# Optimization experiments

Hardware: AMD Instinct MI355X
Metric: run time of the kernel (lower is better)

The kernel has to match this reference:

```python
import jax, jax.numpy as jnp
import numpy as np

THRESHOLD = 0.5
MAX_POINTS = 10000
NORMALIZE = True
BIDIRECTIONAL = True
INF = jnp.float32(1e30)


def _voxels_to_points(vox):
    # vox: (D, H, W). Returns padded points (MAX_POINTS, 3) and validity mask.
    D, H, W = vox.shape
    flat = vox.reshape(-1)
    active = flat > THRESHOLD
    n_active = jnp.sum(active.astype(jnp.int32))
    # Stable argsort puts active voxel indices first (deterministic stand-in
    # for torch's randperm subsampling when n_active > MAX_POINTS).
    order = jnp.argsort(jnp.where(active, 0, 1).astype(jnp.int32))
    idx = order[:MAX_POINTS]
    valid = jnp.arange(MAX_POINTS) < jnp.minimum(n_active, MAX_POINTS)
    d = idx // (H * W)
    h = (idx // W) % H
    w = idx % W
    pts = jnp.stack([d, h, w], axis=-1).astype(jnp.float32)  # (MAX_POINTS, 3)
    if NORMALIZE:
        pts = pts / (D - 1) * 2.0 - 1.0
    pts = jnp.where(valid[:, None], pts, 0.0)
    return pts, valid


def _chamfer_single(p1, v1, p2, v2):
    # p1: (N,3), p2: (M,3) padded; v1/v2 are validity masks.
    n1 = jnp.sum(p1 * p1, axis=1)  # (N,)
    n2 = jnp.sum(p2 * p2, axis=1)  # (M,)
    dist = n1[:, None] + n2[None, :] - 2.0 * (p1 @ p2.T)  # (N, M)
    dist = jnp.maximum(dist, 0.0)
    c1 = jnp.maximum(jnp.sum(v1.astype(jnp.float32)), 1.0)
    c2 = jnp.maximum(jnp.sum(v2.astype(jnp.float32)), 1.0)
    min_1to2 = jnp.min(jnp.where(v2[None, :], dist, INF), axis=1)  # (N,)
    loss = jnp.sum(jnp.where(v1, min_1to2, 0.0)) / c1
    if BIDIRECTIONAL:
        min_2to1 = jnp.min(jnp.where(v1[:, None], dist, INF), axis=0)  # (M,)
        loss = loss + jnp.sum(jnp.where(v2, min_2to1, 0.0)) / c2
    return loss


def setup_inputs() -> dict:
    key = jax.random.key(0)
    k1, k2 = jax.random.split(key)
    pred = jax.random.uniform(k1, (4, 1, 64, 64, 64), dtype=jnp.float32)
    target = jax.random.uniform(k2, (4, 1, 64, 64, 64), dtype=jnp.float32)
    return {"pred": pred, "target": target}


def reference(pred, target):
    B = pred.shape[0]
    total = jnp.float32(0.0)
    n_valid = jnp.float32(0.0)
    for b in range(B):  # small fixed batch loop (per-sample dist matrix is 10k x 10k)
        p1, v1 = _voxels_to_points(pred[b, 0])
        p2, v2 = _voxels_to_points(target[b, 0])
        has_pts = jnp.logical_and(jnp.any(v1), jnp.any(v2))
        cd = _chamfer_single(p1, v1, p2, v2)
        total = total + jnp.where(has_pts, cd, 0.0)
        n_valid = n_valid + has_pts.astype(jnp.float32)
    return jnp.where(n_valid > 0, total / jnp.maximum(n_valid, 1.0), 0.0)
```

## Files before the change

kernel.cpp:

```cpp
#include <hip/hip_runtime.h>
#include <hip/hip_bf16.h>


#define NVOX      262144
#define NCHUNK    256
#define MAXPTS    10000
#define PTS_PAD   10240
#define NCLOUD    8
#define NTASK     8
#define NRB       40
#define QPB       256
#define NQB       40
#define RSPLIT    4
#define RLEN      2560
#define CH_REFS   1280
#define CH_STEPS  20
#define NCH       2
#define SCALE     (2.0f/63.0f)

typedef _Float16 half8  __attribute__((ext_vector_type(8)));
typedef float    f32x16 __attribute__((ext_vector_type(16)));

#define WS_TOTALS   0
#define WS_COUNTS   1024
#define WS_OFFSETS  16384
#define WS_QFRAG    32768
#define WS_RFRAG    1343488
#define WS_NQ       2654208
#define WS_SMIN     2981888
#define WS_BSUM     4292608

__device__ __forceinline__ const float* cloud_src(const float* pred, const float* tgt, int cloud) {
    const float* base = (cloud & 1) ? tgt : pred;
    return base + (size_t)(cloud >> 1) * NVOX;
}

__global__ void k_init(half8* __restrict__ Qfrag, half8* __restrict__ Rfrag,
                       float* __restrict__ nqint) {
    int i = blockIdx.x * 256 + threadIdx.x;
    half8 zq = {0, 0, 0, 0, 0, 0, 0, 0};
    half8 zr = {0, 0, 0, (_Float16)4096, 0, 0, 0, 0};
    Qfrag[i] = zq;
    Rfrag[i] = zr;
    nqint[i] = 0.f;
}

__global__ void k_count(const float* __restrict__ pred, const float* __restrict__ tgt,
                        int* __restrict__ counts) {
    int cloud = blockIdx.x >> 8;
    int chunk = blockIdx.x & 255;
    int t = threadIdx.x;
    const float* src = cloud_src(pred, tgt, cloud) + chunk * 1024;
    float4 v = reinterpret_cast<const float4*>(src)[t];
    int cnt = (v.x > 0.5f) + (v.y > 0.5f) + (v.z > 0.5f) + (v.w > 0.5f);
    __shared__ int s[256];
    s[t] = cnt; __syncthreads();
    for (int o = 128; o > 0; o >>= 1) {
        if (t < o) s[t] += s[t + o];
        __syncthreads();
    }
    if (t == 0) counts[cloud * NCHUNK + chunk] = s[0];
}

__global__ void k_scan(const int* __restrict__ counts, int* __restrict__ offsets,
                       int* __restrict__ totals) {
    int cloud = blockIdx.x;
    int t = threadIdx.x;
    int c = counts[cloud * NCHUNK + t];
    __shared__ int s[256];
    s[t] = c; __syncthreads();
    for (int o = 1; o < 256; o <<= 1) {
        int v = (t >= o) ? s[t - o] : 0;
        __syncthreads();
        s[t] += v;
        __syncthreads();
    }
    offsets[cloud * NCHUNK + t] = s[t] - c;
    if (t == 255) totals[cloud] = s[255];
}

__global__ void k_compact(const float* __restrict__ pred, const float* __restrict__ tgt,
                          const int* __restrict__ offsets,
                          half8* __restrict__ Qfrag, half8* __restrict__ Rfrag,
                          float* __restrict__ nqint) {
    int cloud = blockIdx.x >> 8;
    int chunk = blockIdx.x & 255;
    int t = threadIdx.x;
    const float* src = cloud_src(pred, tgt, cloud) + chunk * 1024;
    float4 v = reinterpret_cast<const float4*>(src)[t];
    int f0 = v.x > 0.5f, f1 = v.y > 0.5f, f2 = v.z > 0.5f, f3 = v.w > 0.5f;
    int cnt = f0 + f1 + f2 + f3;
    __shared__ int s[256];
    s[t] = cnt; __syncthreads();
    for (int o = 1; o < 256; o <<= 1) {
        int x = (t >= o) ? s[t - o] : 0;
        __syncthreads();
        s[t] += x;
        __syncthreads();
    }
    int rank = offsets[cloud * NCHUNK + chunk] + (s[t] - cnt);
    int eidx = chunk * 1024 + t * 4;
    int flags[4] = {f0, f1, f2, f3};
    size_t base = (size_t)cloud * PTS_PAD;
    #pragma unroll
    for (int e = 0; e < 4; ++e) {
        if (flags[e]) {
            if (rank < MAXPTS) {
                int idx = eidx + e;
                int d = idx >> 12, h = (idx >> 6) & 63, w = idx & 63;
                int nr = d * d + h * h + w * w;
                half8 Q = {(_Float16)(-2 * d), (_Float16)(-2 * h), (_Float16)(-2 * w),
                           (_Float16)8, (_Float16)1, 0, 0, 0};
                half8 R = {(_Float16)d, (_Float16)h, (_Float16)w,
                           (_Float16)(nr >> 3), (_Float16)(nr & 7), 0, 0, 0};
                Qfrag[base + rank] = Q;
                Rfrag[base + rank] = R;
                nqint[base + rank] = (float)nr;
            }
            rank++;
        }
    }
}

__device__ __forceinline__ float mintree(f32x16 d0, f32x16 d1, float m) {
    float t[4];
    #pragma unroll
    for (int e = 0; e < 4; ++e) {
        float u = fminf(fminf(d0[e], d0[e + 4]), d0[e + 8]);
        u = fminf(fminf(u, d0[e + 12]), d1[e]);
        u = fminf(fminf(u, d1[e + 4]), d1[e + 8]);
        u = fminf(u, d1[e + 12]);
        t[e] = u;
    }
    return fminf(fminf(m, fminf(t[0], t[1])), fminf(t[2], t[3]));
}

__global__ __launch_bounds__(256, 3) void k_chamfer(const half8* __restrict__ Qfrag,
                                                    const half8* __restrict__ Rfrag,
                                                    float* __restrict__ smin) {
    int task = blockIdx.x / (NQB * RSPLIT);
    int rem  = blockIdx.x % (NQB * RSPLIT);
    int qb   = rem / RSPLIT;
    int rs   = rem % RSPLIT;
    int b = task >> 1, dir = task & 1;
    int qc = 2 * b + dir;
    int rc = 2 * b + (dir ^ 1);
    int tid = threadIdx.x, wave = tid >> 6, lane = tid & 63;

    __shared__ float4 ldsv[CH_REFS];
    char* lds = (char*)ldsv;

    int qbase = qb * QPB + wave * 64;
    half8 zero8 = {0, 0, 0, 0, 0, 0, 0, 0};
    half8 bq0 = zero8, bq1 = zero8;
    if (lane < 32) {
        bq0 = Qfrag[(size_t)qc * PTS_PAD + qbase + lane];
        bq1 = Qfrag[(size_t)qc * PTS_PAD + qbase + 32 + lane];
    }
    float m0 = 1e30f, m1 = 1e30f;
    f32x16 cz;
    #pragma unroll
    for (int e = 0; e < 16; ++e) cz[e] = 0.f;

    const float4* Rsrc = (const float4*)(Rfrag + (size_t)rc * PTS_PAD + rs * RLEN);
    const char* rdbase = lds + (lane & 31) * 16;

    for (int c = 0; c < NCH; ++c) {
        __syncthreads();
        const float4* src = Rsrc + c * CH_REFS;
        #pragma unroll
        for (int i = 0; i < CH_REFS / 256; ++i) ldsv[tid + i * 256] = src[tid + i * 256];
        __syncthreads();
        #pragma unroll 2
        for (int t = 0; t < CH_STEPS; ++t) {
            half8 a0 = *(const half8*)(rdbase + t * 1024);
            half8 a1 = *(const half8*)(rdbase + t * 1024 + 512);
            f32x16 d0 = __builtin_amdgcn_mfma_f32_32x32x16_f16(a0, bq0, cz, 0, 0, 0);
            f32x16 d1 = __builtin_amdgcn_mfma_f32_32x32x16_f16(a1, bq0, cz, 0, 0, 0);
            f32x16 d2 = __builtin_amdgcn_mfma_f32_32x32x16_f16(a0, bq1, cz, 0, 0, 0);
            f32x16 d3 = __builtin_amdgcn_mfma_f32_32x32x16_f16(a1, bq1, cz, 0, 0, 0);
            m0 = mintree(d0, d1, m0);
            m1 = mintree(d2, d3, m1);
        }
    }

    m0 = fminf(m0, __shfl_xor(m0, 32));
    m1 = fminf(m1, __shfl_xor(m1, 32));
    if (lane < 32) {
        float* outp = smin + ((size_t)task * RSPLIT + rs) * PTS_PAD + qbase;
        outp[lane] = m0;
        outp[32 + lane] = m1;
    }
}

__global__ void k_reduce(const float* __restrict__ nqint, const int* __restrict__ totals,
                         const float* __restrict__ smin, float* __restrict__ bsum) {
    int task = blockIdx.x / NRB;
    int rb   = blockIdx.x % NRB;
    int tid  = threadIdx.x;
    int qi   = rb * 256 + tid;
    int qc   = 2 * (task >> 1) + (task & 1);
    int countQ = min(totals[qc], MAXPTS);

    const float SC2 = SCALE * SCALE;
    float contrib = 0.f;
    if (qi < countQ) {
        const float* s = smin + (size_t)task * RSPLIT * PTS_PAD + qi;
        float m = fminf(fminf(s[0], s[PTS_PAD]), fminf(s[2 * PTS_PAD], s[3 * PTS_PAD]));
        float nq = nqint[(size_t)qc * PTS_PAD + qi];
        contrib = fmaxf((nq + m) * SC2, 0.f);
    }
    __shared__ float sb[256];
    sb[tid] = contrib; __syncthreads();
    for (int o = 128; o > 0; o >>= 1) {
        if (tid < o) sb[tid] += sb[tid + o];
        __syncthreads();
    }
    if (tid == 0) bsum[task * NRB + rb] = sb[0];
}

__global__ void k_final(const float* __restrict__ bsum, const int* __restrict__ totals,
                        float* __restrict__ out) {
    float total = 0.f, nv = 0.f;
    for (int b = 0; b < 4; ++b) {
        float s1 = 0.f, s2 = 0.f;
        for (int i = 0; i < NRB; ++i) {
            s1 += bsum[(2 * b) * NRB + i];
            s2 += bsum[(2 * b + 1) * NRB + i];
        }
        int c1 = min(totals[2 * b], MAXPTS);
        int c2 = min(totals[2 * b + 1], MAXPTS);
        float cd = s1 / fmaxf((float)c1, 1.f) + s2 / fmaxf((float)c2, 1.f);
        if (c1 > 0 && c2 > 0) { total += cd; nv += 1.f; }
    }
    out[0] = (nv > 0.f) ? total / nv : 0.f;
}

extern "C" void kernel_launch(void* const* d_in, const int* in_sizes, int n_in,
                              void* d_out, int out_size, void* d_ws, size_t ws_size,
                              hipStream_t stream) {
    const float* pred = (const float*)d_in[0];
    const float* tgt  = (const float*)d_in[1];
    float* out = (float*)d_out;

    char* ws = (char*)d_ws;
    int*   totals  = (int*)(ws + WS_TOTALS);
    int*   counts  = (int*)(ws + WS_COUNTS);
    int*   offsets = (int*)(ws + WS_OFFSETS);
    half8* Qfrag   = (half8*)(ws + WS_QFRAG);
    half8* Rfrag   = (half8*)(ws + WS_RFRAG);
    float* nqint   = (float*)(ws + WS_NQ);
    float* smin    = (float*)(ws + WS_SMIN);
    float* bsum    = (float*)(ws + WS_BSUM);

    k_init   <<<NCLOUD * PTS_PAD / 256, 256, 0, stream>>>(Qfrag, Rfrag, nqint);
    k_count  <<<NCLOUD * NCHUNK, 256, 0, stream>>>(pred, tgt, counts);
    k_scan   <<<NCLOUD,          256, 0, stream>>>(counts, offsets, totals);
    k_compact<<<NCLOUD * NCHUNK, 256, 0, stream>>>(pred, tgt, offsets, Qfrag, Rfrag, nqint);
    k_chamfer<<<NTASK * NQB * RSPLIT, 256, 0, stream>>>(Qfrag, Rfrag, smin);
    k_reduce <<<NTASK * NRB,     256, 0, stream>>>(nqint, totals, smin, bsum);
    k_final  <<<1, 1, 0, stream>>>(bsum, totals, out);
}
```

Measured before the change: 51.42 us.

## Widen chamfer query tile, split references further, fuse init into count

```diff
diff --git a/kernel.cpp b/kernel.cpp
--- a/kernel.cpp
+++ b/kernel.cpp
@@ -9,12 +9,12 @@
 #define NCLOUD    8
 #define NTASK     8
 #define NRB       40
-#define QPB       256
-#define NQB       40
-#define RSPLIT    4
-#define RLEN      2560
-#define CH_REFS   1280
-#define CH_STEPS  20
+#define QPB       512
+#define NQB       20
+#define RSPLIT    8
+#define RLEN      1280
+#define CH_REFS   640
+#define CH_STEPS  10
 #define NCH       2
 #define SCALE     (2.0f/63.0f)
 
@@ -28,25 +28,25 @@
 #define WS_RFRAG    1343488
 #define WS_NQ       2654208
 #define WS_SMIN     2981888
-#define WS_BSUM     4292608
+#define WS_BSUM     5603328
 
 __device__ __forceinline__ const float* cloud_src(const float* pred, const float* tgt, int cloud) {
     const float* base = (cloud & 1) ? tgt : pred;
     return base + (size_t)(cloud >> 1) * NVOX;
 }
 
-__global__ void k_init(half8* __restrict__ Qfrag, half8* __restrict__ Rfrag,
-                       float* __restrict__ nqint) {
-    int i = blockIdx.x * 256 + threadIdx.x;
-    half8 zq = {0, 0, 0, 0, 0, 0, 0, 0};
-    half8 zr = {0, 0, 0, (_Float16)4096, 0, 0, 0, 0};
-    Qfrag[i] = zq;
-    Rfrag[i] = zr;
-    nqint[i] = 0.f;
-}
-
 __global__ void k_count(const float* __restrict__ pred, const float* __restrict__ tgt,
-                        int* __restrict__ counts) {
+                        int* __restrict__ counts,
+                        half8* __restrict__ Qfrag, half8* __restrict__ Rfrag,
+                        float* __restrict__ nqint) {
+    int gi = blockIdx.x * 256 + threadIdx.x;
+    if (gi < NCLOUD * PTS_PAD) {
+        half8 zq = {0, 0, 0, 0, 0, 0, 0, 0};
+        half8 zr = {0, 0, 0, (_Float16)4096, 0, 0, 0, 0};
+        Qfrag[gi] = zq;
+        Rfrag[gi] = zr;
+        nqint[gi] = 0.f;
+    }
     int cloud = blockIdx.x >> 8;
     int chunk = blockIdx.x & 255;
     int t = threadIdx.x;
@@ -122,20 +122,26 @@
     }
 }
 
-__device__ __forceinline__ float mintree(f32x16 d0, f32x16 d1, float m) {
-    float t[4];
-    #pragma unroll
-    for (int e = 0; e < 4; ++e) {
-        float u = fminf(fminf(d0[e], d0[e + 4]), d0[e + 8]);
-        u = fminf(fminf(u, d0[e + 12]), d1[e]);
-        u = fminf(fminf(u, d1[e + 4]), d1[e + 8]);
-        u = fminf(u, d1[e + 12]);
-        t[e] = u;
-    }
-    return fminf(fminf(m, fminf(t[0], t[1])), fminf(t[2], t[3]));
-}
-
-__global__ __launch_bounds__(256, 3) void k_chamfer(const half8* __restrict__ Qfrag,
+__device__ __forceinline__ float red16(f32x16 d, float m) {
+    float t0 = fminf(fminf(d[0], d[1]), d[2]);
+    float t1 = fminf(fminf(d[3], d[4]), d[5]);
+    float t2 = fminf(fminf(d[6], d[7]), d[8]);
+    float t3 = fminf(fminf(d[9], d[10]), d[11]);
+    float t4 = fminf(fminf(d[12], d[13]), d[14]);
+    float t5 = fminf(d[15], m);
+    float u0 = fminf(fminf(t0, t1), t2);
+    float u1 = fminf(fminf(t3, t4), t5);
+    return fminf(u0, u1);
+}
+
+#define MFMA_MIN(aa, bb, mm)                                                      \
+    do {                                                                          \
+        f32x16 d_ = __builtin_amdgcn_mfma_f32_32x32x16_f16((aa), (bb), cz, 0, 0, 0); \
+        asm("" : "+v"(d_));                                                       \
+        (mm) = red16(d_, (mm));                                                   \
+    } while (0)
+
+__global__ __launch_bounds__(256, 4) void k_chamfer(const half8* __restrict__ Qfrag,
                                                     const half8* __restrict__ Rfrag,
                                                     float* __restrict__ smin) {
     int task = blockIdx.x / (NQB * RSPLIT);
@@ -150,14 +156,14 @@
     __shared__ float4 ldsv[CH_REFS];
     char* lds = (char*)ldsv;
 
-    int qbase = qb * QPB + wave * 64;
+    int qbase = qb * QPB + wave * 128;
     half8 zero8 = {0, 0, 0, 0, 0, 0, 0, 0};
-    half8 bq0 = zero8, bq1 = zero8;
+    half8 bq0 = zero8, bq1 = zero8, bq2 = zero8, bq3 = zero8;
     if (lane < 32) {
-        bq0 = Qfrag[(size_t)qc * PTS_PAD + qbase + lane];
-        bq1 = Qfrag[(size_t)qc * PTS_PAD + qbase + 32 + lane];
-    }
-    float m0 = 1e30f, m1 = 1e30f;
+        const half8* qp = Qfrag + (size_t)qc * PTS_PAD + qbase + lane;
+        bq0 = qp[0]; bq1 = qp[32]; bq2 = qp[64]; bq3 = qp[96];
+    }
+    float m0 = 1e30f, m1 = 1e30f, m2 = 1e30f, m3 = 1e30f;
     f32x16 cz;
     #pragma unroll
     for (int e = 0; e < 16; ++e) cz[e] = 0.f;
@@ -168,28 +174,33 @@
     for (int c = 0; c < NCH; ++c) {
         __syncthreads();
         const float4* src = Rsrc + c * CH_REFS;
-        #pragma unroll
-        for (int i = 0; i < CH_REFS / 256; ++i) ldsv[tid + i * 256] = src[tid + i * 256];
+        for (int i = tid; i < CH_REFS; i += 256) ldsv[i] = src[i];
         __syncthreads();
         #pragma unroll 2
         for (int t = 0; t < CH_STEPS; ++t) {
             half8 a0 = *(const half8*)(rdbase + t * 1024);
             half8 a1 = *(const half8*)(rdbase + t * 1024 + 512);
-            f32x16 d0 = __builtin_amdgcn_mfma_f32_32x32x16_f16(a0, bq0, cz, 0, 0, 0);
-            f32x16 d1 = __builtin_amdgcn_mfma_f32_32x32x16_f16(a1, bq0, cz, 0, 0, 0);
-            f32x16 d2 = __builtin_amdgcn_mfma_f32_32x32x16_f16(a0, bq1, cz, 0, 0, 0);
-            f32x16 d3 = __builtin_amdgcn_mfma_f32_32x32x16_f16(a1, bq1, cz, 0, 0, 0);
-            m0 = mintree(d0, d1, m0);
-            m1 = mintree(d2, d3, m1);
+            MFMA_MIN(a0, bq0, m0);
+            MFMA_MIN(a1, bq0, m0);
+            MFMA_MIN(a0, bq1, m1);
+            MFMA_MIN(a1, bq1, m1);
+            MFMA_MIN(a0, bq2, m2);
+            MFMA_MIN(a1, bq2, m2);
+            MFMA_MIN(a0, bq3, m3);
+            MFMA_MIN(a1, bq3, m3);
         }
     }
 
     m0 = fminf(m0, __shfl_xor(m0, 32));
     m1 = fminf(m1, __shfl_xor(m1, 32));
+    m2 = fminf(m2, __shfl_xor(m2, 32));
+    m3 = fminf(m3, __shfl_xor(m3, 32));
     if (lane < 32) {
-        float* outp = smin + ((size_t)task * RSPLIT + rs) * PTS_PAD + qbase;
-        outp[lane] = m0;
-        outp[32 + lane] = m1;
+        float* outp = smin + ((size_t)task * RSPLIT + rs) * PTS_PAD + qbase + lane;
+        outp[0]  = m0;
+        outp[32] = m1;
+        outp[64] = m2;
+        outp[96] = m3;
     }
 }
 
@@ -206,7 +217,10 @@
     float contrib = 0.f;
     if (qi < countQ) {
         const float* s = smin + (size_t)task * RSPLIT * PTS_PAD + qi;
-        float m = fminf(fminf(s[0], s[PTS_PAD]), fminf(s[2 * PTS_PAD], s[3 * PTS_PAD]));
+        float m = fminf(fminf(s[0 * PTS_PAD], s[1 * PTS_PAD]),
+                        fminf(s[2 * PTS_PAD], s[3 * PTS_PAD]));
+        m = fminf(m, fminf(fminf(s[4 * PTS_PAD], s[5 * PTS_PAD]),
+                           fminf(s[6 * PTS_PAD], s[7 * PTS_PAD])));
         float nq = nqint[(size_t)qc * PTS_PAD + qi];
         contrib = fmaxf((nq + m) * SC2, 0.f);
     }
@@ -253,8 +267,7 @@
     float* smin    = (float*)(ws + WS_SMIN);
     float* bsum    = (float*)(ws + WS_BSUM);
 
-    k_init   <<<NCLOUD * PTS_PAD / 256, 256, 0, stream>>>(Qfrag, Rfrag, nqint);
-    k_count  <<<NCLOUD * NCHUNK, 256, 0, stream>>>(pred, tgt, counts);
+    k_count  <<<NCLOUD * NCHUNK, 256, 0, stream>>>(pred, tgt, counts, Qfrag, Rfrag, nqint);
     k_scan   <<<NCLOUD,          256, 0, stream>>>(counts, offsets, totals);
     k_compact<<<NCLOUD * NCHUNK, 256, 0, stream>>>(pred, tgt, offsets, Qfrag, Rfrag, nqint);
     k_chamfer<<<NTASK * NQB * RSPLIT, 256, 0, stream>>>(Qfrag, Rfrag, smin);
```

Result: faster. 48.34 us (-6.0%).
